# Kernel optimization log

Measured on AMD Instinct MI355X. Metric: run time of the kernel, lower is better.

## Reference

```python
import jax, jax.numpy as jnp
import numpy as np

CAPACITY = 1_000_000
IN_FEATURES = 64
OUT_FEATURES = 64


def setup_inputs() -> dict:
    key = jax.random.key(0)
    k1, k2, k3 = jax.random.split(key, 3)
    query = jax.random.normal(k1, (IN_FEATURES,), dtype=jnp.float32)
    keys = jax.random.normal(k2, (CAPACITY, IN_FEATURES), dtype=jnp.float32)
    values = jax.random.normal(k3, (CAPACITY, OUT_FEATURES), dtype=jnp.float32)
    return {"query": query, "keys": keys, "values": values}


def reference(query, keys, values):
    # attention: [capacity] = keys [C, Din] @ query [Din]
    scores = keys @ query
    attention = jax.nn.softmax(scores, axis=0)
    # out: [Dout] = attention [C] @ values [C, Dout]
    out = attention @ values
    # usage-tracking argmax (softmax is monotone, argmax of scores == argmax of attention)
    amax = jnp.argmax(scores)
    return out, amax
```

## Files before the change

### kernel.cpp

```cpp
#include <hip/hip_runtime.h>
#include <math.h>

#define C_CAP 1000000
#define DIM 64

#define SCORES_OFF 0
#define P1_OFF     1000000
#define HDR_OFF    1010000
#define ACC_OFF    1010064

#define NB1 2048
#define NTILES (C_CAP / 16)
#define NCHUNKS (C_CAP / 64)

__global__ __launch_bounds__(256, 8) void nd_scores(
    const float* __restrict__ query,
    const float* __restrict__ keys,
    float* __restrict__ ws, int ntiles, int nwaves_total)
{
    const int tid  = threadIdx.x;
    const int lane = tid & 63;
    const int wave = tid >> 6;
    const int cl   = lane & 15;
    const int g    = lane >> 4;
    const int wglobal = blockIdx.x * 4 + wave;

    const float4 q4 = ((const float4*)query)[cl];
    const float4* __restrict__ k4p = (const float4*)keys;

    float m = -1e30f, l = 0.f;
    int idx = 0;

    for (int t = wglobal; t < ntiles; t += nwaves_total) {
        const float4* __restrict__ kp = k4p + (size_t)t * 256 + lane;
        float4 k[4];
        #pragma unroll
        for (int j = 0; j < 4; ++j) k[j] = kp[j * 64];

        float s[4];
        #pragma unroll
        for (int j = 0; j < 4; ++j) {
            s[j] = fmaf(k[j].x, q4.x,
                   fmaf(k[j].y, q4.y,
                   fmaf(k[j].z, q4.z, k[j].w * q4.w)));
        }
        #pragma unroll
        for (int off = 1; off <= 8; off <<= 1) {
            #pragma unroll
            for (int j = 0; j < 4; ++j) s[j] += __shfl_xor(s[j], off);
        }

        const float sv = (cl == 0) ? s[0] : (cl == 1) ? s[1]
                       : (cl == 2) ? s[2] : s[3];
        if (cl < 4) ws[SCORES_OFF + t * 16 + 4 * cl + g] = sv;

        float p[4];
        #pragma unroll
        for (int j = 0; j < 4; ++j) p[j] = __expf(s[j]);
        l += (p[0] + p[1]) + (p[2] + p[3]);

        const int rbase = t * 16 + g;
        #pragma unroll
        for (int j = 0; j < 4; ++j) {
            if (s[j] > m) { m = s[j]; idx = rbase + 4 * j; }
        }
    }

    #pragma unroll
    for (int off = 16; off <= 32; off <<= 1) {
        l += __shfl_xor(l, off);
        const float mo = __shfl_xor(m, off);
        const int  io  = __shfl_xor(idx, off);
        if (mo > m) { m = mo; idx = io; }
    }

    __shared__ float s_m[4], s_l[4];
    __shared__ int   s_idx[4];
    if (lane == 0) { s_m[wave] = m; s_l[wave] = l; s_idx[wave] = idx; }
    __syncthreads();
    if (tid == 0) {
        float bm = s_m[0], bl = s_l[0]; int bi = s_idx[0];
        #pragma unroll
        for (int wv = 1; wv < 4; ++wv) {
            bl += s_l[wv];
            if (s_m[wv] > bm) { bm = s_m[wv]; bi = s_idx[wv]; }
        }
        float* bp = ws + P1_OFF + (size_t)blockIdx.x * 4;
        bp[0] = bm;
        bp[1] = bl;
        ((int*)bp)[2] = bi;
    }
}

__global__ __launch_bounds__(256) void nd_reduce(float* __restrict__ ws, int nb)
{
    const int tid = threadIdx.x;
    float m = -1e30f, l = 0.f; int idx = 0;
    for (int b = tid; b < nb; b += 256) {
        const float* bp = ws + P1_OFF + (size_t)b * 4;
        l += bp[1];
        if (bp[0] > m) { m = bp[0]; idx = ((const int*)bp)[2]; }
    }
    __shared__ float sm[256], sl[256];
    __shared__ int   si[256];
    sm[tid] = m; sl[tid] = l; si[tid] = idx;
    __syncthreads();
    for (int s = 128; s > 0; s >>= 1) {
        if (tid < s) {
            sl[tid] += sl[tid + s];
            if (sm[tid + s] > sm[tid]) { sm[tid] = sm[tid + s]; si[tid] = si[tid + s]; }
        }
        __syncthreads();
    }
    if (tid == 0) {
        const float M = sm[0];
        ws[HDR_OFF + 0] = M;
        ws[HDR_OFF + 1] = sl[0] * __expf(-M);
        ((int*)ws)[HDR_OFF + 2] = si[0];
    }
    if (tid < 64) ws[ACC_OFF + tid] = 0.f;
}

__global__ __launch_bounds__(256, 8) void nd_pv(
    const float* __restrict__ values,
    float* __restrict__ ws, int nchunks, int nwaves_total)
{
    const int tid  = threadIdx.x;
    const int lane = tid & 63;
    const int wave = tid >> 6;
    const int wglobal = blockIdx.x * 4 + wave;

    const float M = ws[HDR_OFF];
    float acc = 0.f;

    for (int c = wglobal; c < nchunks; c += nwaves_total) {
        const float s = ws[SCORES_OFF + (size_t)c * 64 + lane];
        const float w = __expf(s - M);
        unsigned long long mask = __ballot(w > 1e-10f);
        while (mask) {
            const int b = __ffsll((long long)mask) - 1;
            mask &= mask - 1;
            const float wb = __shfl(w, b);
            acc = fmaf(wb, values[(size_t)(c * 64 + b) * 64 + lane], acc);
        }
    }

    __shared__ float sA[4][64];
    sA[wave][lane] = acc;
    __syncthreads();
    if (tid < 64) {
        const float v = sA[0][tid] + sA[1][tid] + sA[2][tid] + sA[3][tid];
        if (v != 0.f) atomicAdd(ws + ACC_OFF + tid, v);
    }
}

__global__ __launch_bounds__(128) void nd_final(
    const float* __restrict__ ws, float* __restrict__ out)
{
    const int tid = threadIdx.x;
    if (tid < 64) out[tid] = ws[ACC_OFF + tid] / ws[HDR_OFF + 1];
    if (tid == 64) out[64] = (float)((const int*)ws)[HDR_OFF + 2];
}

extern "C" void kernel_launch(void* const* d_in, const int* in_sizes, int n_in,
                              void* d_out, int out_size, void* d_ws, size_t ws_size,
                              hipStream_t stream) {
    const float* query  = (const float*)d_in[0];
    const float* keys   = (const float*)d_in[1];
    const float* values = (const float*)d_in[2];
    float* out = (float*)d_out;
    float* ws  = (float*)d_ws;

    const int nwaves = NB1 * 4;

    nd_scores<<<NB1, 256, 0, stream>>>(query, keys, ws, NTILES, nwaves);
    nd_reduce<<<1, 256, 0, stream>>>(ws, NB1);
    nd_pv<<<NB1, 256, 0, stream>>>(values, ws, NCHUNKS, nwaves);
    nd_final<<<1, 128, 0, stream>>>(ws, out);
}
```

Before: 482.1 us.

## Fold reduce and final kernels into last-block epilogues and prefetch key tiles

Removes the single-block reduce and final kernels. Blocks now publish partials with atomics and bump a counter, and the last block to finish does the global max/sum/argmax reduction or the output normalization. The scores loop also software-prefetches the next key tile into registers before computing the current one. This saves two kernel launches and their serialization gaps and hides load latency, at the cost of a memset launch, counter atomics and higher register pressure.

After: 698.9 us. 45.0% more time.

```diff
diff --git a/kernel.cpp b/kernel.cpp
--- a/kernel.cpp
+++ b/kernel.cpp
@@ -8,15 +8,17 @@
 #define P1_OFF     1000000
 #define HDR_OFF    1010000
 #define ACC_OFF    1010064
+#define CNT_OFF    1010176
 
 #define NB1 2048
 #define NTILES (C_CAP / 16)
 #define NCHUNKS (C_CAP / 64)
+#define NWAVES (NB1 * 4)
 
 __global__ __launch_bounds__(256, 8) void nd_scores(
     const float* __restrict__ query,
     const float* __restrict__ keys,
-    float* __restrict__ ws, int ntiles, int nwaves_total)
+    float* __restrict__ ws)
 {
     const int tid  = threadIdx.x;
     const int lane = tid & 63;
@@ -31,19 +33,28 @@
     float m = -1e30f, l = 0.f;
     int idx = 0;
 
-    for (int t = wglobal; t < ntiles; t += nwaves_total) {
+    int t = wglobal;
+    float4 kc[4];
+    if (t < NTILES) {
         const float4* __restrict__ kp = k4p + (size_t)t * 256 + lane;
-        float4 k[4];
-        #pragma unroll
-        for (int j = 0; j < 4; ++j) k[j] = kp[j * 64];
+        #pragma unroll
+        for (int j = 0; j < 4; ++j) kc[j] = kp[j * 64];
+    }
+    while (t < NTILES) {
+        const int tn = t + NWAVES;
+        float4 kn[4];
+        if (tn < NTILES) {
+            const float4* __restrict__ kp = k4p + (size_t)tn * 256 + lane;
+            #pragma unroll
+            for (int j = 0; j < 4; ++j) kn[j] = kp[j * 64];
+        }
 
         float s[4];
         #pragma unroll
-        for (int j = 0; j < 4; ++j) {
-            s[j] = fmaf(k[j].x, q4.x,
-                   fmaf(k[j].y, q4.y,
-                   fmaf(k[j].z, q4.z, k[j].w * q4.w)));
-        }
+        for (int j = 0; j < 4; ++j)
+            s[j] = fmaf(kc[j].x, q4.x,
+                   fmaf(kc[j].y, q4.y,
+                   fmaf(kc[j].z, q4.z, kc[j].w * q4.w)));
         #pragma unroll
         for (int off = 1; off <= 8; off <<= 1) {
             #pragma unroll
@@ -52,18 +63,20 @@
 
         const float sv = (cl == 0) ? s[0] : (cl == 1) ? s[1]
                        : (cl == 2) ? s[2] : s[3];
-        if (cl < 4) ws[SCORES_OFF + t * 16 + 4 * cl + g] = sv;
-
-        float p[4];
-        #pragma unroll
-        for (int j = 0; j < 4; ++j) p[j] = __expf(s[j]);
-        l += (p[0] + p[1]) + (p[2] + p[3]);
+        if (cl < 4) ws[SCORES_OFF + (size_t)t * 16 + 4 * cl + g] = sv;
+
+        const float p0 = __expf(s[0]), p1 = __expf(s[1]);
+        const float p2 = __expf(s[2]), p3 = __expf(s[3]);
+        l += (p0 + p1) + (p2 + p3);
 
         const int rbase = t * 16 + g;
         #pragma unroll
-        for (int j = 0; j < 4; ++j) {
+        for (int j = 0; j < 4; ++j)
             if (s[j] > m) { m = s[j]; idx = rbase + 4 * j; }
-        }
+
+        t = tn;
+        #pragma unroll
+        for (int j = 0; j < 4; ++j) kc[j] = kn[j];
     }
 
     #pragma unroll
@@ -76,6 +89,7 @@
 
     __shared__ float s_m[4], s_l[4];
     __shared__ int   s_idx[4];
+    __shared__ int   s_last;
     if (lane == 0) { s_m[wave] = m; s_l[wave] = l; s_idx[wave] = idx; }
     __syncthreads();
     if (tid == 0) {
@@ -86,44 +100,49 @@
             if (s_m[wv] > bm) { bm = s_m[wv]; bi = s_idx[wv]; }
         }
         float* bp = ws + P1_OFF + (size_t)blockIdx.x * 4;
-        bp[0] = bm;
-        bp[1] = bl;
-        ((int*)bp)[2] = bi;
-    }
-}
-
-__global__ __launch_bounds__(256) void nd_reduce(float* __restrict__ ws, int nb)
-{
-    const int tid = threadIdx.x;
-    float m = -1e30f, l = 0.f; int idx = 0;
-    for (int b = tid; b < nb; b += 256) {
+        __hip_atomic_store(bp + 0, bm, __ATOMIC_RELAXED, __HIP_MEMORY_SCOPE_AGENT);
+        __hip_atomic_store(bp + 1, bl, __ATOMIC_RELAXED, __HIP_MEMORY_SCOPE_AGENT);
+        __hip_atomic_store((int*)bp + 2, bi, __ATOMIC_RELAXED, __HIP_MEMORY_SCOPE_AGENT);
+        unsigned* cnt = (unsigned*)(ws + CNT_OFF);
+        const unsigned prev = __hip_atomic_fetch_add(
+            cnt, 1u, __ATOMIC_ACQ_REL, __HIP_MEMORY_SCOPE_AGENT);
+        s_last = (prev == NB1 - 1);
+    }
+    __syncthreads();
+    if (!s_last) return;
+
+    float rm = -1e30f, rl = 0.f; int ri = 0;
+    for (int b = tid; b < NB1; b += 256) {
         const float* bp = ws + P1_OFF + (size_t)b * 4;
-        l += bp[1];
-        if (bp[0] > m) { m = bp[0]; idx = ((const int*)bp)[2]; }
-    }
-    __shared__ float sm[256], sl[256];
-    __shared__ int   si[256];
-    sm[tid] = m; sl[tid] = l; si[tid] = idx;
-    __syncthreads();
-    for (int s = 128; s > 0; s >>= 1) {
-        if (tid < s) {
-            sl[tid] += sl[tid + s];
-            if (sm[tid + s] > sm[tid]) { sm[tid] = sm[tid + s]; si[tid] = si[tid + s]; }
+        const float bm = __hip_atomic_load(bp + 0, __ATOMIC_RELAXED, __HIP_MEMORY_SCOPE_AGENT);
+        const float bl = __hip_atomic_load(bp + 1, __ATOMIC_RELAXED, __HIP_MEMORY_SCOPE_AGENT);
+        const int   bi = __hip_atomic_load((const int*)bp + 2, __ATOMIC_RELAXED, __HIP_MEMORY_SCOPE_AGENT);
+        rl += bl;
+        if (bm > rm) { rm = bm; ri = bi; }
+    }
+    __shared__ float rsm[256], rsl[256];
+    __shared__ int   rsi[256];
+    rsm[tid] = rm; rsl[tid] = rl; rsi[tid] = ri;
+    __syncthreads();
+    for (int st = 128; st > 0; st >>= 1) {
+        if (tid < st) {
+            rsl[tid] += rsl[tid + st];
+            if (rsm[tid + st] > rsm[tid]) { rsm[tid] = rsm[tid + st]; rsi[tid] = rsi[tid + st]; }
         }
         __syncthreads();
     }
     if (tid == 0) {
-        const float M = sm[0];
+        const float M = rsm[0];
         ws[HDR_OFF + 0] = M;
-        ws[HDR_OFF + 1] = sl[0] * __expf(-M);
-        ((int*)ws)[HDR_OFF + 2] = si[0];
+        ws[HDR_OFF + 1] = rsl[0] * __expf(-M);
+        ((int*)ws)[HDR_OFF + 2] = rsi[0];
     }
     if (tid < 64) ws[ACC_OFF + tid] = 0.f;
 }
 
 __global__ __launch_bounds__(256, 8) void nd_pv(
     const float* __restrict__ values,
-    float* __restrict__ ws, int nchunks, int nwaves_total)
+    float* __restrict__ ws, float* __restrict__ out)
 {
     const int tid  = threadIdx.x;
     const int lane = tid & 63;
@@ -133,7 +152,7 @@
     const float M = ws[HDR_OFF];
     float acc = 0.f;
 
-    for (int c = wglobal; c < nchunks; c += nwaves_total) {
+    for (int c = wglobal; c < NCHUNKS; c += NWAVES) {
         const float s = ws[SCORES_OFF + (size_t)c * 64 + lane];
         const float w = __expf(s - M);
         unsigned long long mask = __ballot(w > 1e-10f);
@@ -141,24 +160,34 @@
             const int b = __ffsll((long long)mask) - 1;
             mask &= mask - 1;
             const float wb = __shfl(w, b);
-            acc = fmaf(wb, values[(size_t)(c * 64 + b) * 64 + lane], acc);
+            acc = fmaf(wb, values[((size_t)c * 64 + b) * 64 + lane], acc);
         }
     }
 
     __shared__ float sA[4][64];
+    __shared__ int   s_last;
     sA[wave][lane] = acc;
     __syncthreads();
     if (tid < 64) {
         const float v = sA[0][tid] + sA[1][tid] + sA[2][tid] + sA[3][tid];
         if (v != 0.f) atomicAdd(ws + ACC_OFF + tid, v);
     }
-}
-
-__global__ __launch_bounds__(128) void nd_final(
-    const float* __restrict__ ws, float* __restrict__ out)
-{
-    const int tid = threadIdx.x;
-    if (tid < 64) out[tid] = ws[ACC_OFF + tid] / ws[HDR_OFF + 1];
+    __threadfence();
+    __syncthreads();
+    if (tid == 0) {
+        unsigned* cnt = (unsigned*)(ws + CNT_OFF) + 1;
+        const unsigned prev = __hip_atomic_fetch_add(
+            cnt, 1u, __ATOMIC_ACQ_REL, __HIP_MEMORY_SCOPE_AGENT);
+        s_last = (prev == NB1 - 1);
+    }
+    __syncthreads();
+    if (!s_last) return;
+
+    if (tid < 64) {
+        const float a = __hip_atomic_load(ws + ACC_OFF + tid,
+                                          __ATOMIC_RELAXED, __HIP_MEMORY_SCOPE_AGENT);
+        out[tid] = a / ws[HDR_OFF + 1];
+    }
     if (tid == 64) out[64] = (float)((const int*)ws)[HDR_OFF + 2];
 }
 
@@ -171,10 +200,8 @@
     float* out = (float*)d_out;
     float* ws  = (float*)d_ws;
 
-    const int nwaves = NB1 * 4;
-
-    nd_scores<<<NB1, 256, 0, stream>>>(query, keys, ws, NTILES, nwaves);
-    nd_reduce<<<1, 256, 0, stream>>>(ws, NB1);
-    nd_pv<<<NB1, 256, 0, stream>>>(values, ws, NCHUNKS, nwaves);
-    nd_final<<<1, 128, 0, stream>>>(ws, out);
+    hipMemsetAsync((char*)d_ws + (size_t)CNT_OFF * sizeof(float), 0, 8, stream);
+
+    nd_scores<<<NB1, 256, 0, stream>>>(query, keys, ws);
+    nd_pv<<<NB1, 256, 0, stream>>>(values, ws, out);
 }
```
